# Kernel optimization log

Hardware: AMD Instinct MI355X
Metric: run time of the kernel (lower is better)

## Reference

```python
import jax, jax.numpy as jnp
import numpy as np

B, DC, DB, DF = 16384, 2048, 768, 256
NF = DB  # num_features (isSwinT=True)
EPS = 1e-5


def setup_inputs() -> dict:
    key = jax.random.key(0)
    ks = jax.random.split(key, 20)
    s = 0.02
    return {
        'x_context': jax.random.normal(ks[0], (B, DC), jnp.float32),
        'x_body': jax.random.normal(ks[1], (B, DB), jnp.float32),
        'x_face': jax.random.normal(ks[2], (B, DF), jnp.float32),
        'Wc': jax.random.normal(ks[3], (NF, DC), jnp.float32) * s,
        'bc': jax.random.normal(ks[4], (NF,), jnp.float32) * s,
        'Wa1': jax.random.normal(ks[5], (128, NF), jnp.float32) * s,
        'ba1': jax.random.normal(ks[6], (128,), jnp.float32) * s,
        'ga': jnp.ones((128,), jnp.float32),
        'bba': jnp.zeros((128,), jnp.float32),
        'Wa2': jax.random.normal(ks[7], (1, 128), jnp.float32) * s,
        'ba2': jax.random.normal(ks[8], (1,), jnp.float32) * s,
        'W1': jax.random.normal(ks[9], (256, NF * 3), jnp.float32) * s,
        'b1': jax.random.normal(ks[10], (256,), jnp.float32) * s,
        'g1': jnp.ones((256,), jnp.float32),
        'be1': jnp.zeros((256,), jnp.float32),
        'Wcat': jax.random.normal(ks[11], (26, 256), jnp.float32) * s,
        'bcat': jax.random.normal(ks[12], (26,), jnp.float32) * s,
    }


def _bn(x, g, b):
    # BatchNorm1d, training mode (biased batch stats), deterministic
    m = jnp.mean(x, axis=0)
    v = jnp.mean((x - m) ** 2, axis=0)
    return (x - m) * jax.lax.rsqrt(v + EPS) * g + b


def reference(x_context, x_body, x_face, Wc, bc, Wa1, ba1, ga, bba, Wa2, ba2,
              W1, b1, g1, be1, Wcat, bcat):
    # face repeated elementwise to body width: [B,256,1]->repeat(3)->view[B,768]
    face = jnp.repeat(x_face, DB // DF, axis=1)              # [B, NF]
    ctx = x_context @ Wc.T + bc                              # [B, NF]
    body = x_body                                            # [B, NF]

    def cross_atten(a, u, v):
        # two 1x1 dot-products, softmax over size-2 dim, weighted sum
        d = jnp.stack([jnp.sum(a * u, axis=1), jnp.sum(a * v, axis=1)], axis=1)  # [B,2]
        att = jax.nn.softmax(d, axis=1)
        # sum over dim2 of a[:, :, None] @ att[:, None, :] == a * att.sum(1)
        return a * jnp.sum(att, axis=1, keepdims=True)

    cfeat = cross_atten(ctx, body, face)
    bfeat = cross_atten(body, ctx, face)
    ffeat = cross_atten(face, ctx, body)

    def fc_att(x):
        h = _bn(x @ Wa1.T + ba1, ga, bba)
        h = jax.nn.gelu(h, approximate=False)
        return h @ Wa2.T + ba2                               # [B, 1]

    score = jax.nn.softmax(
        jnp.concatenate([fc_att(cfeat), fc_att(bfeat), fc_att(ffeat)], axis=1), axis=1)  # [B,3]
    cfeat = cfeat * score[:, 0:1]
    bfeat = bfeat * score[:, 1:2]
    ffeat = ffeat * score[:, 2:3]

    fuse = jnp.concatenate([cfeat, bfeat, ffeat], axis=1) @ W1.T + b1  # [B,256]
    fuse = jax.nn.relu(_bn(fuse, g1, be1))  # dropout p=0.5 treated as identity (eval)
    return fuse @ Wcat.T + bcat             # [B,26]
```

## Files before the change

kernel.cpp:

```cpp
#include <hip/hip_runtime.h>
#include <hip/hip_bf16.h>
#include <stdint.h>

typedef float f32x4 __attribute__((ext_vector_type(4)));
typedef short bf16x8 __attribute__((ext_vector_type(8)));
typedef unsigned short u16;

static constexpr int kB  = 16384;
static constexpr int kDC = 2048;
static constexpr int kNF = 768;
static constexpr float kEps = 1e-5f;

static constexpr size_t OFF_FEATS  = 0;
static constexpr size_t OFF_X      = 75497472;
static constexpr size_t OFF_WCBF   = OFF_X + 67108864;
static constexpr size_t OFF_WA1BF  = OFF_WCBF + 3145728;
static constexpr size_t OFF_W1BF   = OFF_WA1BF + 196608;
static constexpr size_t OFF_FUSE   = OFF_W1BF + 1179648;
static constexpr size_t OFF_SCORES = OFF_FUSE + 16777216;
static constexpr size_t OFF_STATS  = OFF_SCORES + 196608;

static __device__ __forceinline__ u16 f2bf(float x) {
  union { float f; unsigned u; } c; c.f = x;
  unsigned r = c.u + 0x7fffu + ((c.u >> 16) & 1u);
  return (u16)(r >> 16);
}

static __device__ __forceinline__ void cvt4(const float* __restrict__ in, u16* __restrict__ out, long v) {
  const float4 f = ((const float4*)in)[v];
  ((ushort4*)out)[v] = make_ushort4(f2bf(f.x), f2bf(f.y), f2bf(f.z), f2bf(f.w));
}

__global__ __launch_bounds__(256) void prep_kernel(
    const float* __restrict__ xc, const float* __restrict__ xb, const float* __restrict__ xf,
    const float* __restrict__ Wc, const float* __restrict__ Wa1, const float* __restrict__ W1,
    u16* __restrict__ axbf, u16* __restrict__ feats,
    u16* __restrict__ wcbf, u16* __restrict__ wa1bf, u16* __restrict__ w1bf)
{
  const int b = blockIdx.x, t = threadIdx.x;
  if (b < 4096) {
    const long base = (long)b * 2048 + t;
#pragma unroll
    for (int i = 0; i < 8; ++i) cvt4(xc, axbf, base + i * 256);
  } else if (b < 5632) {
    const long base = (long)(b - 4096) * 2048 + t;
    u16* o = feats + (size_t)kB * kNF;
#pragma unroll
    for (int i = 0; i < 8; ++i) cvt4(xb, o, base + i * 256);
  } else if (b < 6144) {
    const long base = (long)(b - 5632) * 2048 + t;
#pragma unroll
    for (int i = 0; i < 8; ++i) {
      const long v = base + i * 256;
      const float4 f = ((const float4*)xf)[v];
      u16 e0 = f2bf(f.x), e1 = f2bf(f.y), e2 = f2bf(f.z), e3 = f2bf(f.w);
      size_t p = (size_t)v * 4;
      size_t row = p >> 8;
      int col = (int)(p & 255);
      u16* o = feats + (size_t)2 * kB * kNF + row * kNF + col * 3;
      ushort4* o4 = (ushort4*)o;
      o4[0] = make_ushort4(e0, e0, e0, e1);
      o4[1] = make_ushort4(e1, e1, e2, e2);
      o4[2] = make_ushort4(e2, e3, e3, e3);
    }
  } else if (b < 6336) {
    const long base = (long)(b - 6144) * 2048 + t;
#pragma unroll
    for (int i = 0; i < 8; ++i) cvt4(Wc, wcbf, base + i * 256);
  } else if (b < 6348) {
    const long base = (long)(b - 6336) * 2048 + t;
#pragma unroll
    for (int i = 0; i < 8; ++i) cvt4(Wa1, wa1bf, base + i * 256);
  } else {
    const long base = (long)(b - 6348) * 2048 + t;
#pragma unroll
    for (int i = 0; i < 8; ++i) cvt4(W1, w1bf, base + i * 256);
  }
}

static __device__ __forceinline__ void gload16(const void* g, void* l) {
  __builtin_amdgcn_global_load_lds(
      (const __attribute__((address_space(1))) void*)g,
      (__attribute__((address_space(3))) void*)l, 16, 0, 0);
}

__global__ __launch_bounds__(256) void gemm_bt(
    const u16* __restrict__ A, int lda, const u16* __restrict__ B, int ldb,
    const float* __restrict__ bias, u16* __restrict__ C, int ldc, int K)
{
  __shared__ __align__(16) u16 As[128 * 32];
  __shared__ __align__(16) u16 Bs[128 * 32];
  const int bx = blockIdx.x, by = blockIdx.y;
  const size_t m0 = (size_t)bx * 128;
  const int n0 = by * 128;
  const int t = threadIdx.x;
  const int lane = t & 63, wave = t >> 6;
  const int wm = (wave >> 1) * 64, wn = (wave & 1) * 64;
  const int fr = lane & 15, fq = lane >> 4;

  const int srow = t >> 2, scol = (t & 3) * 8;
  const u16* ga0 = A + (m0 + srow) * (size_t)lda + scol;
  const u16* ga1 = A + (m0 + 64 + srow) * (size_t)lda + scol;
  const u16* gb0 = B + (size_t)(n0 + srow) * ldb + scol;
  const u16* gb1 = B + (size_t)(n0 + 64 + srow) * ldb + scol;
  u16* la = As + t * 8;
  u16* lb = Bs + t * 8;
  const u16* fa = As + (wm + fr) * 32 + fq * 8;
  const u16* fb = Bs + (wn + fr) * 32 + fq * 8;

  f32x4 acc[4][4] = {};

  const int kt = K >> 5;
  for (int k = 0; k < kt; ++k) {
    __syncthreads();
    gload16(ga0, la);
    gload16(ga1, la + 2048);
    gload16(gb0, lb);
    gload16(gb1, lb + 2048);
    ga0 += 32; ga1 += 32; gb0 += 32; gb1 += 32;
    __syncthreads();
    bf16x8 av[4], bv[4];
#pragma unroll
    for (int mf = 0; mf < 4; ++mf) av[mf] = *(const bf16x8*)(fa + mf * 512);
#pragma unroll
    for (int nf = 0; nf < 4; ++nf) bv[nf] = *(const bf16x8*)(fb + nf * 512);
#pragma unroll
    for (int mf = 0; mf < 4; ++mf)
#pragma unroll
      for (int nf = 0; nf < 4; ++nf)
        acc[mf][nf] = __builtin_amdgcn_mfma_f32_16x16x32_bf16(av[mf], bv[nf], acc[mf][nf], 0, 0, 0);
  }

#pragma unroll
  for (int mf = 0; mf < 4; ++mf) {
    const size_t rb = m0 + wm + mf * 16 + fq * 4;
#pragma unroll
    for (int nf = 0; nf < 4; ++nf) {
      const int gn = n0 + wn + nf * 16 + fr;
      const float bb = bias[gn];
#pragma unroll
      for (int rr = 0; rr < 4; ++rr)
        C[(rb + rr) * (size_t)ldc + gn] = f2bf(acc[mf][nf][rr] + bb);
    }
  }
}

template <int STATS>
__global__ __launch_bounds__(256) void gemm_bt64(
    const u16* __restrict__ A, int lda, const u16* __restrict__ B, int ldb,
    const float* __restrict__ bias, float* __restrict__ C, int ldc, int K,
    float* __restrict__ stats)
{
  __shared__ __align__(16) u16 As[2 * 64 * 32];
  __shared__ __align__(16) u16 Bs[2 * 128 * 32];
  const int bx = blockIdx.x, by = blockIdx.y;
  const size_t m0 = (size_t)bx * 64;
  const int n0 = by * 128;
  const int t = threadIdx.x;
  const int lane = t & 63, wave = t >> 6;
  const int wn = wave * 32;
  const int fr = lane & 15, fq = lane >> 4;

  const int srow = t >> 2, scol = (t & 3) * 8;
  const u16* ga0 = A + (m0 + srow) * (size_t)lda + scol;
  const u16* gb0 = B + (size_t)(n0 + srow) * ldb + scol;
  const u16* gb1 = B + (size_t)(n0 + 64 + srow) * ldb + scol;

  f32x4 acc[4][2] = {};

  gload16(ga0, As + t * 8);
  gload16(gb0, Bs + t * 8);
  gload16(gb1, Bs + t * 8 + 2048);
  ga0 += 32; gb0 += 32; gb1 += 32;
  __syncthreads();

  const int kt = K >> 5;
  for (int k = 0; k < kt; ++k) {
    const int cur = k & 1;
    if (k + 1 < kt) {
      u16* an = As + (cur ^ 1) * 2048;
      u16* bn = Bs + (cur ^ 1) * 4096;
      gload16(ga0, an + t * 8);
      gload16(gb0, bn + t * 8);
      gload16(gb1, bn + t * 8 + 2048);
      ga0 += 32; gb0 += 32; gb1 += 32;
    }
    const u16* fa = As + cur * 2048 + fr * 32 + fq * 8;
    const u16* fb = Bs + cur * 4096 + (wn + fr) * 32 + fq * 8;
    bf16x8 av[4], bv[2];
#pragma unroll
    for (int mf = 0; mf < 4; ++mf) av[mf] = *(const bf16x8*)(fa + mf * 512);
#pragma unroll
    for (int nf = 0; nf < 2; ++nf) bv[nf] = *(const bf16x8*)(fb + nf * 512);
#pragma unroll
    for (int mf = 0; mf < 4; ++mf)
#pragma unroll
      for (int nf = 0; nf < 2; ++nf)
        acc[mf][nf] = __builtin_amdgcn_mfma_f32_16x16x32_bf16(av[mf], bv[nf], acc[mf][nf], 0, 0, 0);
    __syncthreads();
  }

  float cs[2] = {}, cs2[2] = {};
#pragma unroll
  for (int mf = 0; mf < 4; ++mf) {
    const size_t rb = m0 + mf * 16 + fq * 4;
#pragma unroll
    for (int nf = 0; nf < 2; ++nf) {
      const int gn = n0 + wn + nf * 16 + fr;
      const float bb = bias[gn];
#pragma unroll
      for (int rr = 0; rr < 4; ++rr) {
        const float vv = acc[mf][nf][rr] + bb;
        C[(rb + rr) * (size_t)ldc + gn] = vv;
        if (STATS) { cs[nf] += vv; cs2[nf] += vv * vv; }
      }
    }
  }
  if (STATS) {
    const int f = (int)(m0 >> 14);
#pragma unroll
    for (int nf = 0; nf < 2; ++nf) {
      float s = cs[nf], s2 = cs2[nf];
      s += __shfl_down(s, 32); s2 += __shfl_down(s2, 32);
      s += __shfl_down(s, 16); s2 += __shfl_down(s2, 16);
      if (fq == 0) {
        const int gn = n0 + wn + nf * 16 + fr;
        atomicAdd(&stats[(f * 128 + gn) * 2 + 0], s);
        atomicAdd(&stats[(f * 128 + gn) * 2 + 1], s2);
      }
    }
  }
}

__global__ __launch_bounds__(256) void gemm_fuse64(
    const u16* __restrict__ feats, const u16* __restrict__ w1,
    const float* __restrict__ scores, const float* __restrict__ b1,
    float* __restrict__ fuse, float* __restrict__ fstats)
{
  __shared__ __align__(16) u16 As[2 * 64 * 32];
  __shared__ __align__(16) u16 Bs[2 * 128 * 32];
  const int bx = blockIdx.x, by = blockIdx.y;
  const size_t m0 = (size_t)bx * 64;
  const int n0 = by * 128;
  const int t = threadIdx.x;
  const int lane = t & 63, wave = t >> 6;
  const int wn = wave * 32;
  const int fr = lane & 15, fq = lane >> 4;
  const int srow = t >> 2, scol = (t & 3) * 8;

  const u16* ga0; const u16* gb0; const u16* gb1;
  auto setf = [&](int f) {
    ga0 = feats + (size_t)f * kB * kNF + (m0 + srow) * (size_t)kNF + scol;
    gb0 = w1 + f * kNF + (size_t)(n0 + srow) * 2304 + scol;
    gb1 = gb0 + (size_t)64 * 2304;
  };

  const f32x4 vzero = {};
  f32x4 acc[4][2] = {}, tot[4][2] = {};

  setf(0);
  gload16(ga0, As + t * 8);
  gload16(gb0, Bs + t * 8);
  gload16(gb1, Bs + t * 8 + 2048);
  ga0 += 32; gb0 += 32; gb1 += 32;
  int pf = 0, pk = 1;
  int ck = 0, cf = 0;
  __syncthreads();

  for (int s = 0; s < 72; ++s) {
    const int cur = s & 1;
    if (s < 71) {
      u16* an = As + (cur ^ 1) * 2048;
      u16* bn = Bs + (cur ^ 1) * 4096;
      gload16(ga0, an + t * 8);
      gload16(gb0, bn + t * 8);
      gload16(gb1, bn + t * 8 + 2048);
      if (++pk == 24) { pk = 0; ++pf; if (pf < 3) setf(pf); }
      else { ga0 += 32; gb0 += 32; gb1 += 32; }
    }
    const u16* fa = As + cur * 2048 + fr * 32 + fq * 8;
    const u16* fb = Bs + cur * 4096 + (wn + fr) * 32 + fq * 8;
    bf16x8 av[4], bv[2];
#pragma unroll
    for (int mf = 0; mf < 4; ++mf) av[mf] = *(const bf16x8*)(fa + mf * 512);
#pragma unroll
    for (int nf = 0; nf < 2; ++nf) bv[nf] = *(const bf16x8*)(fb + nf * 512);
#pragma unroll
    for (int mf = 0; mf < 4; ++mf)
#pragma unroll
      for (int nf = 0; nf < 2; ++nf)
        acc[mf][nf] = __builtin_amdgcn_mfma_f32_16x16x32_bf16(av[mf], bv[nf], acc[mf][nf], 0, 0, 0);
    if (++ck == 24) {
      ck = 0;
#pragma unroll
      for (int mf = 0; mf < 4; ++mf) {
        const size_t rb = m0 + mf * 16 + fq * 4;
#pragma unroll
        for (int rr = 0; rr < 4; ++rr) {
          const float sv = scores[(rb + rr) * 3 + cf];
#pragma unroll
          for (int nf = 0; nf < 2; ++nf) tot[mf][nf][rr] += sv * acc[mf][nf][rr];
        }
      }
#pragma unroll
      for (int mf = 0; mf < 4; ++mf)
#pragma unroll
        for (int nf = 0; nf < 2; ++nf) acc[mf][nf] = vzero;
      ++cf;
    }
    __syncthreads();
  }

  float cs[2] = {}, cs2[2] = {};
#pragma unroll
  for (int mf = 0; mf < 4; ++mf) {
    const size_t rb = m0 + mf * 16 + fq * 4;
#pragma unroll
    for (int nf = 0; nf < 2; ++nf) {
      const int gn = n0 + wn + nf * 16 + fr;
      const float bb = b1[gn];
#pragma unroll
      for (int rr = 0; rr < 4; ++rr) {
        const float vv = tot[mf][nf][rr] + bb;
        fuse[(rb + rr) * 256 + gn] = vv;
        cs[nf] += vv; cs2[nf] += vv * vv;
      }
    }
  }
#pragma unroll
  for (int nf = 0; nf < 2; ++nf) {
    float s = cs[nf], s2 = cs2[nf];
    s += __shfl_down(s, 32); s2 += __shfl_down(s2, 32);
    s += __shfl_down(s, 16); s2 += __shfl_down(s2, 16);
    if (fq == 0) {
      const int gn = n0 + wn + nf * 16 + fr;
      atomicAdd(&fstats[gn * 2 + 0], s);
      atomicAdd(&fstats[gn * 2 + 1], s2);
    }
  }
}

__global__ __launch_bounds__(64) void att_kernel(
    const float* __restrict__ H, const float* __restrict__ stats,
    const float* __restrict__ ga, const float* __restrict__ bba,
    const float* __restrict__ Wa2, const float* __restrict__ ba2,
    float* __restrict__ scores)
{
  const int i = blockIdx.x, l = threadIdx.x;
  float d[3];
#pragma unroll
  for (int f = 0; f < 3; ++f) {
    float part = 0.f;
#pragma unroll
    for (int h = 0; h < 2; ++h) {
      const int c = l + h * 64;
      const float sum = stats[(f * 128 + c) * 2 + 0];
      const float sq  = stats[(f * 128 + c) * 2 + 1];
      const float m = sum * (1.f / kB);
      const float var = sq * (1.f / kB) - m * m;
      const float rs = rsqrtf(var + kEps);
      const float x = H[((size_t)f * kB + i) * 128 + c];
      const float xn = (x - m) * rs * ga[c] + bba[c];
      const float ge = 0.5f * xn * (1.f + erff(xn * 0.70710678118f));
      part += ge * Wa2[c];
    }
#pragma unroll
    for (int off = 32; off > 0; off >>= 1) part += __shfl_down(part, off);
    d[f] = part;
  }
  if (l == 0) {
    const float b2 = ba2[0];
    float d0 = d[0] + b2, d1 = d[1] + b2, d2 = d[2] + b2;
    const float mx = fmaxf(d0, fmaxf(d1, d2));
    const float e0 = expf(d0 - mx), e1 = expf(d1 - mx), e2 = expf(d2 - mx);
    const float inv = 1.f / (e0 + e1 + e2);
    scores[i * 3 + 0] = e0 * inv;
    scores[i * 3 + 1] = e1 * inv;
    scores[i * 3 + 2] = e2 * inv;
  }
}

__global__ __launch_bounds__(64) void final_kernel(
    const float* __restrict__ fuse, const float* __restrict__ fstats,
    const float* __restrict__ g1, const float* __restrict__ be1,
    const float* __restrict__ Wcat, const float* __restrict__ bcat,
    float* __restrict__ out)
{
  const int i = blockIdx.x, l = threadIdx.x;
  __shared__ float row[256];
#pragma unroll
  for (int h = 0; h < 4; ++h) {
    const int c = l + h * 64;
    const float sum = fstats[c * 2 + 0], sq = fstats[c * 2 + 1];
    const float m = sum * (1.f / kB);
    const float var = sq * (1.f / kB) - m * m;
    const float rs = rsqrtf(var + kEps);
    const float v = (fuse[(size_t)i * 256 + c] - m) * rs * g1[c] + be1[c];
    row[c] = fmaxf(v, 0.f);
  }
  __syncthreads();
  if (l < 26) {
    float acc = bcat[l];
    const float* w = Wcat + l * 256;
    for (int k2 = 0; k2 < 256; ++k2) acc += row[k2] * w[k2];
    out[(size_t)i * 26 + l] = acc;
  }
}

extern "C" void kernel_launch(void* const* d_in, const int* in_sizes, int n_in,
                              void* d_out, int out_size, void* d_ws, size_t ws_size,
                              hipStream_t stream) {
  (void)in_sizes; (void)n_in; (void)out_size; (void)ws_size;
  const float* xc   = (const float*)d_in[0];
  const float* xb   = (const float*)d_in[1];
  const float* xf   = (const float*)d_in[2];
  const float* Wc   = (const float*)d_in[3];
  const float* bc   = (const float*)d_in[4];
  const float* Wa1  = (const float*)d_in[5];
  const float* ba1  = (const float*)d_in[6];
  const float* ga   = (const float*)d_in[7];
  const float* bba  = (const float*)d_in[8];
  const float* Wa2  = (const float*)d_in[9];
  const float* ba2  = (const float*)d_in[10];
  const float* W1   = (const float*)d_in[11];
  const float* b1   = (const float*)d_in[12];
  const float* g1   = (const float*)d_in[13];
  const float* be1  = (const float*)d_in[14];
  const float* Wcat = (const float*)d_in[15];
  const float* bcat = (const float*)d_in[16];
  float* out = (float*)d_out;

  char* ws = (char*)d_ws;
  u16* feats   = (u16*)(ws + OFF_FEATS);
  u16* axbf    = (u16*)(ws + OFF_X);
  float* H     = (float*)(ws + OFF_X);
  u16* wcbf    = (u16*)(ws + OFF_WCBF);
  u16* wa1bf   = (u16*)(ws + OFF_WA1BF);
  u16* w1bf    = (u16*)(ws + OFF_W1BF);
  float* fuse  = (float*)(ws + OFF_FUSE);
  float* scores= (float*)(ws + OFF_SCORES);
  float* hst   = (float*)(ws + OFF_STATS);
  float* fst   = (float*)(ws + OFF_STATS + 3072);

  hipMemsetAsync(ws + OFF_STATS, 0, 5120, stream);
  prep_kernel<<<6420, 256, 0, stream>>>(xc, xb, xf, Wc, Wa1, W1, axbf, feats, wcbf, wa1bf, w1bf);
  gemm_bt<<<dim3(128, 6), 256, 0, stream>>>(axbf, kDC, wcbf, kDC, bc, feats, kNF, kDC);
  gemm_bt64<1><<<dim3(768, 1), 256, 0, stream>>>(feats, kNF, wa1bf, kNF, ba1, H, 128, kNF, hst);
  att_kernel<<<kB, 64, 0, stream>>>(H, hst, ga, bba, Wa2, ba2, scores);
  gemm_fuse64<<<dim3(256, 2), 256, 0, stream>>>(feats, w1bf, scores, b1, fuse, fst);
  final_kernel<<<kB, 64, 0, stream>>>(fuse, fst, g1, be1, Wcat, bcat, out);
}
```

Measured before the change: 300.8 us.

## Move body/face bf16 conversion into context GEMM launch to overlap with compute

The x_body and x_face fp32-to-bf16 conversions move out of the prep kernel and into extra blocks of the context GEMM launch, so that memory-bound conversion work can run alongside the compute-bound GEMM blocks. The conversion helper is also restructured to issue all eight float4 loads before any store, which raises memory-level parallelism. The GEMM is specialised with constant strides and K. The extra conversion blocks run after the GEMM blocks in launch order, so the amount of real overlap depends on how the hardware schedules blocks.

```diff
diff --git a/kernel.cpp b/kernel.cpp
--- a/kernel.cpp
+++ b/kernel.cpp
@@ -26,56 +26,30 @@
   return (u16)(r >> 16);
 }
 
-static __device__ __forceinline__ void cvt4(const float* __restrict__ in, u16* __restrict__ out, long v) {
-  const float4 f = ((const float4*)in)[v];
-  ((ushort4*)out)[v] = make_ushort4(f2bf(f.x), f2bf(f.y), f2bf(f.z), f2bf(f.w));
+static __device__ __forceinline__ void cvt8x4(const float* __restrict__ in,
+                                              u16* __restrict__ out, long base) {
+  float4 f[8];
+#pragma unroll
+  for (int i = 0; i < 8; ++i) f[i] = ((const float4*)in)[base + i * 256];
+#pragma unroll
+  for (int i = 0; i < 8; ++i)
+    ((ushort4*)out)[base + i * 256] =
+        make_ushort4(f2bf(f[i].x), f2bf(f[i].y), f2bf(f[i].z), f2bf(f[i].w));
 }
 
 __global__ __launch_bounds__(256) void prep_kernel(
-    const float* __restrict__ xc, const float* __restrict__ xb, const float* __restrict__ xf,
-    const float* __restrict__ Wc, const float* __restrict__ Wa1, const float* __restrict__ W1,
-    u16* __restrict__ axbf, u16* __restrict__ feats,
-    u16* __restrict__ wcbf, u16* __restrict__ wa1bf, u16* __restrict__ w1bf)
+    const float* __restrict__ xc, const float* __restrict__ Wc,
+    const float* __restrict__ Wa1, const float* __restrict__ W1,
+    u16* __restrict__ axbf, u16* __restrict__ wcbf,
+    u16* __restrict__ wa1bf, u16* __restrict__ w1bf)
 {
   const int b = blockIdx.x, t = threadIdx.x;
-  if (b < 4096) {
-    const long base = (long)b * 2048 + t;
-#pragma unroll
-    for (int i = 0; i < 8; ++i) cvt4(xc, axbf, base + i * 256);
-  } else if (b < 5632) {
-    const long base = (long)(b - 4096) * 2048 + t;
-    u16* o = feats + (size_t)kB * kNF;
-#pragma unroll
-    for (int i = 0; i < 8; ++i) cvt4(xb, o, base + i * 256);
-  } else if (b < 6144) {
-    const long base = (long)(b - 5632) * 2048 + t;
-#pragma unroll
-    for (int i = 0; i < 8; ++i) {
-      const long v = base + i * 256;
-      const float4 f = ((const float4*)xf)[v];
-      u16 e0 = f2bf(f.x), e1 = f2bf(f.y), e2 = f2bf(f.z), e3 = f2bf(f.w);
-      size_t p = (size_t)v * 4;
-      size_t row = p >> 8;
-      int col = (int)(p & 255);
-      u16* o = feats + (size_t)2 * kB * kNF + row * kNF + col * 3;
-      ushort4* o4 = (ushort4*)o;
-      o4[0] = make_ushort4(e0, e0, e0, e1);
-      o4[1] = make_ushort4(e1, e1, e2, e2);
-      o4[2] = make_ushort4(e2, e3, e3, e3);
-    }
-  } else if (b < 6336) {
-    const long base = (long)(b - 6144) * 2048 + t;
-#pragma unroll
-    for (int i = 0; i < 8; ++i) cvt4(Wc, wcbf, base + i * 256);
-  } else if (b < 6348) {
-    const long base = (long)(b - 6336) * 2048 + t;
-#pragma unroll
-    for (int i = 0; i < 8; ++i) cvt4(Wa1, wa1bf, base + i * 256);
-  } else {
-    const long base = (long)(b - 6348) * 2048 + t;
-#pragma unroll
-    for (int i = 0; i < 8; ++i) cvt4(W1, w1bf, base + i * 256);
-  }
+  const float* in; u16* out; long base;
+  if (b < 4096)      { in = xc;  out = axbf;  base = (long)b * 2048 + t; }
+  else if (b < 4288) { in = Wc;  out = wcbf;  base = (long)(b - 4096) * 2048 + t; }
+  else if (b < 4300) { in = Wa1; out = wa1bf; base = (long)(b - 4288) * 2048 + t; }
+  else               { in = W1;  out = w1bf;  base = (long)(b - 4300) * 2048 + t; }
+  cvt8x4(in, out, base);
 }
 
 static __device__ __forceinline__ void gload16(const void* g, void* l) {
@@ -84,25 +58,54 @@
       (__attribute__((address_space(3))) void*)l, 16, 0, 0);
 }
 
-__global__ __launch_bounds__(256) void gemm_bt(
-    const u16* __restrict__ A, int lda, const u16* __restrict__ B, int ldb,
-    const float* __restrict__ bias, u16* __restrict__ C, int ldc, int K)
+__global__ __launch_bounds__(256) void gemm_ctx_conv(
+    const u16* __restrict__ A, const u16* __restrict__ B,
+    const float* __restrict__ bias, u16* __restrict__ C,
+    const float* __restrict__ xb, const float* __restrict__ xf,
+    u16* __restrict__ feats)
 {
   __shared__ __align__(16) u16 As[128 * 32];
   __shared__ __align__(16) u16 Bs[128 * 32];
-  const int bx = blockIdx.x, by = blockIdx.y;
+  const int id = blockIdx.x, t = threadIdx.x;
+
+  if (id >= 768) {
+    const int c = id - 768;
+    if (c < 1536) {
+      cvt8x4(xb, feats + (size_t)kB * kNF, (long)c * 2048 + t);
+    } else {
+      const long base = (long)(c - 1536) * 2048 + t;
+      float4 f[8];
+#pragma unroll
+      for (int i = 0; i < 8; ++i) f[i] = ((const float4*)xf)[base + i * 256];
+#pragma unroll
+      for (int i = 0; i < 8; ++i) {
+        const long v = base + i * 256;
+        u16 e0 = f2bf(f[i].x), e1 = f2bf(f[i].y), e2 = f2bf(f[i].z), e3 = f2bf(f[i].w);
+        size_t p = (size_t)v * 4;
+        size_t row = p >> 8;
+        int col = (int)(p & 255);
+        u16* o = feats + (size_t)2 * kB * kNF + row * kNF + col * 3;
+        ushort4* o4 = (ushort4*)o;
+        o4[0] = make_ushort4(e0, e0, e0, e1);
+        o4[1] = make_ushort4(e1, e1, e2, e2);
+        o4[2] = make_ushort4(e2, e3, e3, e3);
+      }
+    }
+    return;
+  }
+
+  const int bx = id & 127, by = id >> 7;
   const size_t m0 = (size_t)bx * 128;
   const int n0 = by * 128;
-  const int t = threadIdx.x;
   const int lane = t & 63, wave = t >> 6;
   const int wm = (wave >> 1) * 64, wn = (wave & 1) * 64;
   const int fr = lane & 15, fq = lane >> 4;
 
   const int srow = t >> 2, scol = (t & 3) * 8;
-  const u16* ga0 = A + (m0 + srow) * (size_t)lda + scol;
-  const u16* ga1 = A + (m0 + 64 + srow) * (size_t)lda + scol;
-  const u16* gb0 = B + (size_t)(n0 + srow) * ldb + scol;
-  const u16* gb1 = B + (size_t)(n0 + 64 + srow) * ldb + scol;
+  const u16* ga0 = A + (m0 + srow) * (size_t)kDC + scol;
+  const u16* ga1 = A + (m0 + 64 + srow) * (size_t)kDC + scol;
+  const u16* gb0 = B + (size_t)(n0 + srow) * kDC + scol;
+  const u16* gb1 = B + (size_t)(n0 + 64 + srow) * kDC + scol;
   u16* la = As + t * 8;
   u16* lb = Bs + t * 8;
   const u16* fa = As + (wm + fr) * 32 + fq * 8;
@@ -110,8 +113,7 @@
 
   f32x4 acc[4][4] = {};
 
-  const int kt = K >> 5;
-  for (int k = 0; k < kt; ++k) {
+  for (int k = 0; k < 64; ++k) {
     __syncthreads();
     gload16(ga0, la);
     gload16(ga1, la + 2048);
@@ -140,7 +142,7 @@
       const float bb = bias[gn];
 #pragma unroll
       for (int rr = 0; rr < 4; ++rr)
-        C[(rb + rr) * (size_t)ldc + gn] = f2bf(acc[mf][nf][rr] + bb);
+        C[(rb + rr) * (size_t)kNF + gn] = f2bf(acc[mf][nf][rr] + bb);
     }
   }
 }
@@ -443,8 +445,8 @@
   float* fst   = (float*)(ws + OFF_STATS + 3072);
 
   hipMemsetAsync(ws + OFF_STATS, 0, 5120, stream);
-  prep_kernel<<<6420, 256, 0, stream>>>(xc, xb, xf, Wc, Wa1, W1, axbf, feats, wcbf, wa1bf, w1bf);
-  gemm_bt<<<dim3(128, 6), 256, 0, stream>>>(axbf, kDC, wcbf, kDC, bc, feats, kNF, kDC);
+  prep_kernel<<<4372, 256, 0, stream>>>(xc, Wc, Wa1, W1, axbf, wcbf, wa1bf, w1bf);
+  gemm_ctx_conv<<<2816, 256, 0, stream>>>(axbf, wcbf, bc, feats, xb, xf, feats);
   gemm_bt64<1><<<dim3(768, 1), 256, 0, stream>>>(feats, kNF, wa1bf, kNF, ba1, H, 128, kNF, hst);
   att_kernel<<<kB, 64, 0, stream>>>(H, hst, ga, bba, Wa2, ba2, scores);
   gemm_fuse64<<<dim3(256, 2), 256, 0, stream>>>(feats, w1bf, scores, b1, fuse, fst);
```

Result: faster. 290.4 us (-3.5%).
